# Kernel tuning notes

Hardware: AMD Instinct MI355X
Metric: run time of the kernel (lower is better)

The kernel has to match this reference:

```python
import jax, jax.numpy as jnp
import numpy as np

B, V, H = 4, 256, 128
EPS = 1e-5


def setup_inputs() -> dict:
    key = jax.random.key(0)
    ks = jax.random.split(key, 16)
    inp = {
        "h1": jax.random.normal(ks[0], (B, V, H), jnp.float32),
        "h2": jax.random.normal(ks[1], (B, V, H), jnp.float32),
        "e": jax.random.normal(ks[2], (B, V, V, H), jnp.float32),
        "graph": jax.random.randint(ks[3], (B, V, V), 0, 2, jnp.int32),
    }
    scale = 1.0 / np.sqrt(H)
    for i, nm in enumerate(["U1", "U2", "V1", "V2", "A1", "A2", "C"]):
        inp[f"W_{nm}"] = jax.random.normal(ks[4 + i], (H, H), jnp.float32) * scale
        inp[f"b_{nm}"] = jnp.zeros((H,), jnp.float32)
    for nm in ["h1", "h2", "e"]:
        inp[f"g_{nm}"] = jnp.ones((H,), jnp.float32)   # BN gamma
        inp[f"be_{nm}"] = jnp.zeros((H,), jnp.float32)  # BN beta
    return inp


def _lin(x, W, b):
    # torch nn.Linear: x @ W.T + b
    return jnp.einsum('...i,oi->...o', x, W) + b


def _bn(x, g, b):
    # BatchNorm1d with track_running_stats=False: batch stats over flattened leading dims
    sh = x.shape
    x2 = x.reshape(-1, sh[-1])
    m = x2.mean(axis=0)
    v = x2.var(axis=0)  # biased, as torch BN uses for normalization
    return ((x2 - m) * jax.lax.rsqrt(v + EPS) * g + b).reshape(sh)


def reference(h1, h2, e, graph,
              W_U1, b_U1, W_U2, b_U2, W_V1, b_V1, W_V2, b_V2,
              W_A1, b_A1, W_A2, b_A2, W_C, b_C,
              g_h1, be_h1, g_h2, be_h2, g_e, be_e):
    h1_in, h2_in, e_in = h1, h2, e

    Uh1 = _lin(h1, W_U1, b_U1)
    Uh2 = _lin(h2, W_U2, b_U2)
    Vh1 = _lin(h1, W_V1, b_V1)
    Vh2 = _lin(h2, W_V2, b_V2)

    # Wh1[b,i,j,h] = Vh1[b,j,h] + Vh2[b,i,h] ; Wh2 = transpose(1,2) pattern
    Wh1 = Vh1[:, None, :, :] + Vh2[:, :, None, :]
    Wh2 = Vh1[:, :, None, :] + Vh2[:, None, :, :]

    Ah1 = _lin(h1, W_A1, b_A1)
    Ah2 = _lin(h2, W_A2, b_A2)
    Ce = _lin(e, W_C, b_C)
    e_new = Ah1[:, None, :, :] + Ah2[:, :, None, :] + Ce  # B x V x V x H

    gates = jax.nn.sigmoid(e_new)
    gates_T = jax.nn.sigmoid(jnp.transpose(e_new, (0, 2, 1, 3)))

    # aggregation = 'sum' over dim 2 (graph unused for sum)
    h1n = Uh1 + jnp.sum(gates * Wh1, axis=2)
    h2n = Uh2 + jnp.sum(gates_T * Wh2, axis=2)

    h1n = jax.nn.relu(_bn(h1n, g_h1, be_h1))
    h2n = jax.nn.relu(_bn(h2n, g_h2, be_h2))
    e_out = jax.nn.relu(_bn(e_new, g_e, be_e))

    # mode == 'residual'
    return (h1_in + h1n, h2_in + h2n, e_in + e_out)
```

## Files before the change

### kernel.cpp

```cpp
#include <hip/hip_runtime.h>
#include <hip/hip_fp16.h>
#include <math.h>

#define BB 4
#define VV 256
#define HH 128
#define EPS 1e-5f

typedef __attribute__((ext_vector_type(8))) short short8;
typedef __attribute__((ext_vector_type(8))) __bf16 bf16x8;
typedef __attribute__((ext_vector_type(4))) float f32x4;

__device__ __forceinline__ float sigm_(float x) {
    float ex = __builtin_amdgcn_exp2f(-1.44269504f * x);
    return __builtin_amdgcn_rcpf(1.0f + ex);
}

__device__ __forceinline__ bf16x8 as_bf(short8 s) {
    union { short8 s; bf16x8 b; } u; u.s = s; return u.b;
}

__device__ __forceinline__ void split8n(const float4 x0, const float4 x1,
                                        bf16x8& hi, bf16x8& lo) {
    float xs[8] = {x0.x, x0.y, x0.z, x0.w, x1.x, x1.y, x1.z, x1.w};
    #pragma unroll
    for (int i = 0; i < 8; ++i) {
        float x = xs[i];
        __bf16 h = (__bf16)x;
        float r = x - (float)h;
        hi[i] = h;
        lo[i] = (__bf16)r;
    }
}

__global__ __launch_bounds__(256) void k0_splitW(const float* __restrict__ W_C,
                                                 short* __restrict__ Whl) {
    int t = blockIdx.x * 256 + threadIdx.x;
    int lane = t & 63;
    int grp = t >> 6;
    int kstep = grp >> 3, nsub = grp & 7;
    int n = (lane & 15) * 8 + nsub;
    int kb = kstep * 32 + ((lane >> 4) & 3) * 8;
    const float4* src = (const float4*)(W_C + (size_t)n * HH + kb);
    float4 x0 = src[0], x1 = src[1];
    bf16x8 hi, lo;
    split8n(x0, x1, hi, lo);
    union { bf16x8 b; short8 s; } uh, ul;
    uh.b = hi; ul.b = lo;
    short8* dst = (short8*)Whl;
    dst[(size_t)grp * 128 + 0 * 64 + lane] = uh.s;
    dst[(size_t)grp * 128 + 1 * 64 + lane] = ul.s;
}

struct LinArgs {
    const float* x1; const float* x2;
    const float* W[6]; const float* b[6]; const float* b2[6];
    float* out[6]; float* outf[6];
};

__global__ __launch_bounds__(128) void k1_linears(LinArgs a) {
    __shared__ float xs[2][8][HH];
    const int t = threadIdx.x;
    const int r0 = blockIdx.x * 8;
    {
        const float4* s1 = (const float4*)(a.x1 + (size_t)r0 * HH);
        const float4* s2 = (const float4*)(a.x2 + (size_t)r0 * HH);
        float4* d1 = (float4*)&xs[0][0][0];
        float4* d2 = (float4*)&xs[1][0][0];
        #pragma unroll
        for (int p = 0; p < 2; ++p) {
            d1[t + p * 128] = s1[t + p * 128];
            d2[t + p * 128] = s2[t + p * 128];
        }
    }
    __syncthreads();
    const int h = t;
    const int l15h = h >> 3, nsh = h & 7;
    for (int g = 0; g < 6; ++g) {
        const float* W = a.W[g];
        const float (*x)[HH] = (g < 3) ? xs[0] : xs[1];
        float acc[8];
        #pragma unroll
        for (int r = 0; r < 8; ++r) acc[r] = 0.f;
        const float4* Wrow = (const float4*)(W + (size_t)h * HH);
        #pragma unroll 8
        for (int kq = 0; kq < 32; ++kq) {
            float4 w4 = Wrow[kq];
            #pragma unroll
            for (int r = 0; r < 8; ++r) {
                float4 ev = *(const float4*)&x[r][kq * 4];
                acc[r] = fmaf(ev.x, w4.x, acc[r]);
                acc[r] = fmaf(ev.y, w4.y, acc[r]);
                acc[r] = fmaf(ev.z, w4.z, acc[r]);
                acc[r] = fmaf(ev.w, w4.w, acc[r]);
            }
        }
        float bias = a.b[g][h];
        if (a.b2[g]) bias += a.b2[g][h];
        if (a.out[g]) {
            float* O = a.out[g] + (size_t)r0 * HH + h;
            #pragma unroll
            for (int r = 0; r < 8; ++r) O[(size_t)r * HH] = acc[r] + bias;
        }
        if (a.outf[g]) {
            float* Of = a.outf[g];
            #pragma unroll
            for (int r = 0; r < 8; ++r)
                Of[((size_t)(r0 + r) * 16 + l15h) * 8 + nsh] = acc[r] + bias;
        }
    }
}

template<int STOREH>
__global__ __launch_bounds__(512, 4) void k2_main(
    const float* __restrict__ e,
    const short* __restrict__ Whl,
    const float* __restrict__ A1f, const float* __restrict__ A2f,
    const float* __restrict__ V1f, const float* __restrict__ V2f,
    float* __restrict__ e_new32,
    unsigned short* __restrict__ e_newh,
    float* __restrict__ h1acc,
    float* __restrict__ stats)
{
    __shared__ short8 sW[4096];
    __shared__ float red[8][3][8][16];
    const int t = threadIdx.x;
    const int l = t & 63;
    const int w = t >> 6;
    const int l15 = l & 15;
    const int lq = (l >> 4) & 3;
    const int blk = blockIdx.x;
    const int bi = blk >> 1;
    const int jhalf = blk & 1;
    const int b = bi >> 8;
    const int jbase = jhalf * 128 + w * 16;

    const float* pa = e + (size_t)bi * (VV * HH) +
                      (size_t)(jbase + l15) * HH + lq * 8;
    float4 ec[8];
    #pragma unroll
    for (int kstep = 0; kstep < 4; ++kstep) {
        ec[2 * kstep]     = *(const float4*)(pa + kstep * 32);
        ec[2 * kstep + 1] = *(const float4*)(pa + kstep * 32 + 4);
    }

    {
        const short8* src = (const short8*)Whl;
        #pragma unroll
        for (int p = 0; p < 8; ++p) sW[p * 512 + t] = src[p * 512 + t];
    }
    __syncthreads();

    f32x4 acc[8];
    #pragma unroll
    for (int ns = 0; ns < 8; ++ns) acc[ns] = (f32x4){0.f, 0.f, 0.f, 0.f};

    #pragma unroll
    for (int kstep = 0; kstep < 4; ++kstep) {
        bf16x8 ah, al;
        split8n(ec[2 * kstep], ec[2 * kstep + 1], ah, al);
        #pragma unroll
        for (int ns = 0; ns < 8; ++ns) {
            short8 bh = sW[(size_t)(kstep * 8 + ns) * 128 + l];
            short8 bl = sW[(size_t)(kstep * 8 + ns) * 128 + 64 + l];
            acc[ns] = __builtin_amdgcn_mfma_f32_16x16x32_bf16(
                ah, as_bf(bh), acc[ns], 0, 0, 0);
            acc[ns] = __builtin_amdgcn_mfma_f32_16x16x32_bf16(
                ah, as_bf(bl), acc[ns], 0, 0, 0);
            acc[ns] = __builtin_amdgcn_mfma_f32_16x16x32_bf16(
                al, as_bf(bh), acc[ns], 0, 0, 0);
        }
    }

    union f8u { float4 v[2]; float f[8]; };
    f8u a2, v2;
    {
        const float4* p = (const float4*)(A2f + ((size_t)bi * 16 + l15) * 8);
        a2.v[0] = p[0]; a2.v[1] = p[1];
        const float4* q = (const float4*)(V2f + ((size_t)bi * 16 + l15) * 8);
        v2.v[0] = q[0]; v2.v[1] = q[1];
    }
    float h1a[8], es[8], eq[8];
    #pragma unroll
    for (int ns = 0; ns < 8; ++ns) { h1a[ns] = 0.f; es[ns] = 0.f; eq[ns] = 0.f; }

    #pragma unroll
    for (int r = 0; r < 4; ++r) {
        int j = jbase + lq * 4 + r;
        size_t fro = ((size_t)(b * VV + j) * 16 + l15) * 8;
        f8u a1, v1;
        {
            const float4* p = (const float4*)(A1f + fro);
            a1.v[0] = p[0]; a1.v[1] = p[1];
            const float4* q = (const float4*)(V1f + fro);
            v1.v[0] = q[0]; v1.v[1] = q[1];
        }
        size_t obase = ((size_t)bi * VV + j) * HH + l15 * 8;
        float en8[8];
        #pragma unroll
        for (int ns = 0; ns < 8; ++ns) {
            float en = acc[ns][r] + a1.f[ns] + a2.f[ns];
            en8[ns] = en;
            float s = sigm_(en);
            h1a[ns] = fmaf(s, v1.f[ns] + v2.f[ns], h1a[ns]);
            es[ns] += en;
            eq[ns] = fmaf(en, en, eq[ns]);
        }
        if (STOREH) {
            union { __half2 h[4]; uint4 u; } pk;
            pk.h[0] = __floats2half2_rn(en8[0], en8[1]);
            pk.h[1] = __floats2half2_rn(en8[2], en8[3]);
            pk.h[2] = __floats2half2_rn(en8[4], en8[5]);
            pk.h[3] = __floats2half2_rn(en8[6], en8[7]);
            *(uint4*)(e_newh + obase) = pk.u;
        } else {
            float4 s0 = {en8[0], en8[1], en8[2], en8[3]};
            float4 s1 = {en8[4], en8[5], en8[6], en8[7]};
            *(float4*)(e_new32 + obase) = s0;
            *(float4*)(e_new32 + obase + 4) = s1;
        }
    }

    #pragma unroll
    for (int ns = 0; ns < 8; ++ns) {
        h1a[ns] += __shfl_xor(h1a[ns], 16);
        h1a[ns] += __shfl_xor(h1a[ns], 32);
        es[ns]  += __shfl_xor(es[ns], 16);
        es[ns]  += __shfl_xor(es[ns], 32);
        eq[ns]  += __shfl_xor(eq[ns], 16);
        eq[ns]  += __shfl_xor(eq[ns], 32);
    }
    if (l < 16) {
        #pragma unroll
        for (int ns = 0; ns < 8; ++ns) {
            red[w][0][ns][l15] = h1a[ns];
            red[w][1][ns][l15] = es[ns];
            red[w][2][ns][l15] = eq[ns];
        }
    }
    __syncthreads();
    if (t < 128) {
        int ns = t & 7, li = t >> 3;
        float h1t = 0.f, est = 0.f, eqt = 0.f;
        #pragma unroll
        for (int ww = 0; ww < 8; ++ww) {
            h1t += red[ww][0][ns][li];
            est += red[ww][1][ns][li];
            eqt += red[ww][2][ns][li];
        }
        atomicAdd(&h1acc[(size_t)bi * HH + t], h1t);
        atomicAdd(&stats[0 * HH + t], est);
        atomicAdd(&stats[1 * HH + t], eqt);
    }
}

template<int READH>
__global__ __launch_bounds__(256) void k4_pass2(
    float* __restrict__ e_io,
    const unsigned short* __restrict__ e_newh,
    const float* __restrict__ e_in,
    const float* __restrict__ V1, const float* __restrict__ V2,
    const float* __restrict__ g_e, const float* __restrict__ be_e,
    float* __restrict__ h2acc,
    const float* __restrict__ stats)
{
    const int t = threadIdx.x;
    const int h4 = (t & 31) * 4;
    const int jsub = t >> 5;
    const int blk = blockIdx.x;
    const int Iq = blk & 7;
    const int Jt = (blk >> 3) & 31;
    const int b = blk >> 8;
    const int J = Jt * 8 + jsub;
    const int bJ = (b << 8) + J;

    const float inv_n = 1.0f / (float)(BB * VV * VV);
    float sc[4], sh[4];
    #pragma unroll
    for (int c = 0; c < 4; ++c) {
        int h = h4 + c;
        float mean = stats[0 * HH + h] * inv_n;
        float var  = stats[1 * HH + h] * inv_n - mean * mean;
        float rstd = rsqrtf(var + EPS);
        sc[c] = rstd * g_e[h];
        sh[c] = be_e[h] - mean * sc[c];
    }
    float4 vh1 = *(const float4*)(V1 + (size_t)bJ * HH + h4);
    float4 h2a = {0.f, 0.f, 0.f, 0.f};

    const int I0beg = Iq * 32;
    for (int I0 = I0beg; I0 < I0beg + 32; I0 += 4) {
        float4 en[4], ei[4], v2[4];
        size_t off[4];
        #pragma unroll
        for (int u = 0; u < 4; ++u) {
            int I = I0 + u;
            off[u] = ((size_t)((b * VV + I) * VV) + J) * HH + h4;
            if (READH) {
                ushort4 eh = *(const ushort4*)(e_newh + off[u]);
                en[u].x = __half2float(__ushort_as_half(eh.x));
                en[u].y = __half2float(__ushort_as_half(eh.y));
                en[u].z = __half2float(__ushort_as_half(eh.z));
                en[u].w = __half2float(__ushort_as_half(eh.w));
            } else {
                en[u] = *(const float4*)(e_io + off[u]);
            }
            ei[u] = *(const float4*)(e_in + off[u]);
            v2[u] = *(const float4*)(V2 + (size_t)((b << 8) + I) * HH + h4);
        }
        #pragma unroll
        for (int u = 0; u < 4; ++u) {
            float4 r;
            float* enf = (float*)&en[u];
            float* eif = (float*)&ei[u];
            float* v2f = (float*)&v2[u];
            float* rf = (float*)&r;
            float* h2f = (float*)&h2a;
            float* v1f = (float*)&vh1;
            #pragma unroll
            for (int c = 0; c < 4; ++c) {
                float e_ = enf[c];
                h2f[c] = fmaf(sigm_(e_), v1f[c] + v2f[c], h2f[c]);
                float bn = fmaf(e_, sc[c], sh[c]);
                rf[c] = eif[c] + fmaxf(bn, 0.f);
            }
            *(float4*)(e_io + off[u]) = r;
        }
    }
    float* base = h2acc + (size_t)bJ * HH + h4;
    float* h2f = (float*)&h2a;
    #pragma unroll
    for (int c = 0; c < 4; ++c) atomicAdd(base + c, h2f[c]);
}

__global__ __launch_bounds__(256) void k45_combine(
    float* __restrict__ h1acc, float* __restrict__ h2acc,
    const float* __restrict__ U1, const float* __restrict__ U2,
    float* __restrict__ stats)
{
    __shared__ float red[2][2][128];
    const int t = threadIdx.x;
    const int h = t & 127;
    const int rr = t >> 7;
    const int region = blockIdx.x >> 5;
    const int r0 = (blockIdx.x & 31) * 32;
    float* acc = region ? h2acc : h1acc;
    const float* U = region ? U2 : U1;
    float s = 0.f, q = 0.f;
    #pragma unroll
    for (int rs = 0; rs < 16; ++rs) {
        size_t idx = (size_t)(r0 + rr * 16 + rs) * HH + h;
        float v = acc[idx] + U[idx];
        acc[idx] = v;
        s += v;
        q = fmaf(v, v, q);
    }
    red[0][rr][h] = s;
    red[1][rr][h] = q;
    __syncthreads();
    if (t < 128) {
        atomicAdd(&stats[(2 + 2 * region) * HH + h], red[0][0][h] + red[0][1][h]);
        atomicAdd(&stats[(3 + 2 * region) * HH + h], red[1][0][h] + red[1][1][h]);
    }
}

__global__ __launch_bounds__(256) void k5_final(
    const float* __restrict__ h1_in, const float* __restrict__ h2_in,
    const float* __restrict__ h1p, const float* __restrict__ h2p,
    const float* __restrict__ g1, const float* __restrict__ be1,
    const float* __restrict__ g2, const float* __restrict__ be2,
    float* __restrict__ out,
    const float* __restrict__ stats)
{
    const float inv_n = 1.0f / 1024.0f;
    int idx0 = blockIdx.x * 2048 + threadIdx.x;
    #pragma unroll
    for (int p = 0; p < 8; ++p) {
        int idx = idx0 + p * 256;
        int region = idx >> 17;
        int local = idx & 131071;
        int h = idx & 127;
        float ssum = stats[(2 + 2 * region) * HH + h];
        float ssq  = stats[(3 + 2 * region) * HH + h];
        float mean = ssum * inv_n;
        float var  = ssq * inv_n - mean * mean;
        float rstd = rsqrtf(var + EPS);
        const float* g  = region ? g2 : g1;
        const float* be = region ? be2 : be1;
        float sc = rstd * g[h];
        float sh = be[h] - mean * sc;
        const float* xin = region ? h2_in : h1_in;
        const float* pre = region ? h2p : h1p;
        out[idx] = xin[local] + fmaxf(fmaf(pre[local], sc, sh), 0.f);
    }
}

extern "C" void kernel_launch(void* const* d_in, const int* in_sizes, int n_in,
                              void* d_out, int out_size, void* d_ws, size_t ws_size,
                              hipStream_t stream) {
    const float* h1   = (const float*)d_in[0];
    const float* h2   = (const float*)d_in[1];
    const float* e    = (const float*)d_in[2];
    const float* W_U1 = (const float*)d_in[4];
    const float* b_U1 = (const float*)d_in[5];
    const float* W_U2 = (const float*)d_in[6];
    const float* b_U2 = (const float*)d_in[7];
    const float* W_V1 = (const float*)d_in[8];
    const float* b_V1 = (const float*)d_in[9];
    const float* W_V2 = (const float*)d_in[10];
    const float* b_V2 = (const float*)d_in[11];
    const float* W_A1 = (const float*)d_in[12];
    const float* b_A1 = (const float*)d_in[13];
    const float* W_A2 = (const float*)d_in[14];
    const float* b_A2 = (const float*)d_in[15];
    const float* W_C  = (const float*)d_in[16];
    const float* b_C  = (const float*)d_in[17];
    const float* g_h1 = (const float*)d_in[18];
    const float* be_h1= (const float*)d_in[19];
    const float* g_h2 = (const float*)d_in[20];
    const float* be_h2= (const float*)d_in[21];
    const float* g_e  = (const float*)d_in[22];
    const float* be_e = (const float*)d_in[23];

    float* ws = (float*)d_ws;
    const size_t S = (size_t)BB * VV * HH;
    float* U1  = ws + 0 * S;
    float* U2  = ws + 1 * S;
    float* V1  = ws + 2 * S;
    float* V2  = ws + 3 * S;
    float* V1f = ws + 4 * S;
    float* V2f = ws + 5 * S;
    float* A1f = ws + 6 * S;
    float* A2f = ws + 7 * S;
    float* h1acc = ws + 8 * S;
    float* h2acc = ws + 9 * S;
    float* stats = ws + 10 * S;
    short* Whl  = (short*)(stats + 768);
    unsigned short* e_newh = (unsigned short*)(Whl + 32768);

    const size_t EN = (size_t)BB * VV * VV * HH;
    const size_t needed = (10 * S + 768) * 4 + 65536 + EN * 2;
    const bool useh = ws_size >= needed;

    float* out = (float*)d_out;
    float* eo = out + 2 * S;

    hipMemsetAsync(h1acc, 0, (2 * S + 768) * sizeof(float), stream);

    k0_splitW<<<8, 256, 0, stream>>>(W_C, Whl);

    LinArgs la;
    la.x1 = h1; la.x2 = h2;
    la.W[0] = W_U1; la.b[0] = b_U1; la.b2[0] = nullptr; la.out[0] = U1; la.outf[0] = nullptr;
    la.W[1] = W_V1; la.b[1] = b_V1; la.b2[1] = nullptr; la.out[1] = V1; la.outf[1] = V1f;
    la.W[2] = W_A1; la.b[2] = b_A1; la.b2[2] = b_C;     la.out[2] = nullptr; la.outf[2] = A1f;
    la.W[3] = W_U2; la.b[3] = b_U2; la.b2[3] = nullptr; la.out[3] = U2; la.outf[3] = nullptr;
    la.W[4] = W_V2; la.b[4] = b_V2; la.b2[4] = nullptr; la.out[4] = V2; la.outf[4] = V2f;
    la.W[5] = W_A2; la.b[5] = b_A2; la.b2[5] = nullptr; la.out[5] = nullptr; la.outf[5] = A2f;
    k1_linears<<<128, 128, 0, stream>>>(la);

    if (useh) {
        k2_main<1><<<BB * VV * 2, 512, 0, stream>>>(e, Whl, A1f, A2f, V1f, V2f,
                                                    eo, e_newh, h1acc, stats);
        k4_pass2<1><<<BB * 32 * 8, 256, 0, stream>>>(eo, e_newh, e, V1, V2,
                                                     g_e, be_e, h2acc, stats);
    } else {
        k2_main<0><<<BB * VV * 2, 512, 0, stream>>>(e, Whl, A1f, A2f, V1f, V2f,
                                                    eo, e_newh, h1acc, stats);
        k4_pass2<0><<<BB * 32 * 8, 256, 0, stream>>>(eo, e_newh, e, V1, V2,
                                                     g_e, be_e, h2acc, stats);
    }

    k45_combine<<<64, 256, 0, stream>>>(h1acc, h2acc, U1, U2, stats);

    k5_final<<<128, 256, 0, stream>>>(h1, h2, h1acc, h2acc,
                                      g_h1, be_h1, g_h2, be_h2, out, stats);
}
```

Before: 188.3 us.

## Fold memset, weight split and h1 combine into neighbouring kernels

Removes the memset and the separate W_C hi/lo split launch by folding both into the linear-projection kernel, with extra blocks doing the split and every thread doing a grid-stride zero fill. The h1 residual/stat combine moves into spare blocks of the pass-2 kernel, so only the h2 combine remains as its own launch. The k2 MFMA loop also raises wave priority with s_setprio. This cuts launch count and per-launch overhead. The zero fill now runs inside the same kernel as other work that writes elsewhere, so ordering depends only on the kernel boundary before k2.

```diff
diff --git a/kernel.cpp b/kernel.cpp
--- a/kernel.cpp
+++ b/kernel.cpp
@@ -33,35 +33,45 @@
     }
 }
 
-__global__ __launch_bounds__(256) void k0_splitW(const float* __restrict__ W_C,
-                                                 short* __restrict__ Whl) {
-    int t = blockIdx.x * 256 + threadIdx.x;
-    int lane = t & 63;
-    int grp = t >> 6;
-    int kstep = grp >> 3, nsub = grp & 7;
-    int n = (lane & 15) * 8 + nsub;
-    int kb = kstep * 32 + ((lane >> 4) & 3) * 8;
-    const float4* src = (const float4*)(W_C + (size_t)n * HH + kb);
-    float4 x0 = src[0], x1 = src[1];
-    bf16x8 hi, lo;
-    split8n(x0, x1, hi, lo);
-    union { bf16x8 b; short8 s; } uh, ul;
-    uh.b = hi; ul.b = lo;
-    short8* dst = (short8*)Whl;
-    dst[(size_t)grp * 128 + 0 * 64 + lane] = uh.s;
-    dst[(size_t)grp * 128 + 1 * 64 + lane] = ul.s;
-}
-
 struct LinArgs {
     const float* x1; const float* x2;
     const float* W[6]; const float* b[6]; const float* b2[6];
     float* out[6]; float* outf[6];
 };
 
-__global__ __launch_bounds__(128) void k1_linears(LinArgs a) {
+__global__ __launch_bounds__(128) void k1_fused(LinArgs a,
+                                                const float* __restrict__ W_C,
+                                                short* __restrict__ Whl,
+                                                float4* __restrict__ zbase,
+                                                int nz4) {
+    const int blk = blockIdx.x;
+    const int tid = threadIdx.x;
+    {
+        int gtid = blk * 128 + tid;
+        float4 z = {0.f, 0.f, 0.f, 0.f};
+        for (int i = gtid; i < nz4; i += 144 * 128) zbase[i] = z;
+    }
+    if (blk >= 128) {
+        int t = (blk - 128) * 128 + tid;
+        int lane = t & 63;
+        int grp = t >> 6;
+        int kstep = grp >> 3, nsub = grp & 7;
+        int n = (lane & 15) * 8 + nsub;
+        int kb = kstep * 32 + ((lane >> 4) & 3) * 8;
+        const float4* src = (const float4*)(W_C + (size_t)n * HH + kb);
+        float4 x0 = src[0], x1 = src[1];
+        bf16x8 hi, lo;
+        split8n(x0, x1, hi, lo);
+        union { bf16x8 b; short8 s; } uh, ul;
+        uh.b = hi; ul.b = lo;
+        short8* dst = (short8*)Whl;
+        dst[(size_t)grp * 128 + 0 * 64 + lane] = uh.s;
+        dst[(size_t)grp * 128 + 1 * 64 + lane] = ul.s;
+        return;
+    }
     __shared__ float xs[2][8][HH];
-    const int t = threadIdx.x;
-    const int r0 = blockIdx.x * 8;
+    const int t = tid;
+    const int r0 = blk * 8;
     {
         const float4* s1 = (const float4*)(a.x1 + (size_t)r0 * HH);
         const float4* s2 = (const float4*)(a.x2 + (size_t)r0 * HH);
@@ -155,6 +165,7 @@
     #pragma unroll
     for (int ns = 0; ns < 8; ++ns) acc[ns] = (f32x4){0.f, 0.f, 0.f, 0.f};
 
+    __builtin_amdgcn_s_setprio(1);
     #pragma unroll
     for (int kstep = 0; kstep < 4; ++kstep) {
         bf16x8 ah, al;
@@ -171,6 +182,7 @@
                 al, as_bf(bh), acc[ns], 0, 0, 0);
         }
     }
+    __builtin_amdgcn_s_setprio(0);
 
     union f8u { float4 v[2]; float f[8]; };
     f8u a2, v2;
@@ -262,12 +274,39 @@
     const float* __restrict__ V1, const float* __restrict__ V2,
     const float* __restrict__ g_e, const float* __restrict__ be_e,
     float* __restrict__ h2acc,
-    const float* __restrict__ stats)
+    float* __restrict__ h1acc, const float* __restrict__ U1,
+    float* __restrict__ stats)
 {
+    __shared__ float red[2][2][128];
     const int t = threadIdx.x;
+    const int blk = blockIdx.x;
+
+    if (blk >= 1024) {
+        const int rb = blk - 1024;
+        const int h = t & 127;
+        const int rr = t >> 7;
+        const int r0 = rb * 32;
+        float s = 0.f, q = 0.f;
+        #pragma unroll
+        for (int rs = 0; rs < 16; ++rs) {
+            size_t idx = (size_t)(r0 + rr * 16 + rs) * HH + h;
+            float v = h1acc[idx] + U1[idx];
+            h1acc[idx] = v;
+            s += v;
+            q = fmaf(v, v, q);
+        }
+        red[0][rr][h] = s;
+        red[1][rr][h] = q;
+        __syncthreads();
+        if (t < 128) {
+            atomicAdd(&stats[2 * HH + h], red[0][0][h] + red[0][1][h]);
+            atomicAdd(&stats[3 * HH + h], red[1][0][h] + red[1][1][h]);
+        }
+        return;
+    }
+
     const int h4 = (t & 31) * 4;
     const int jsub = t >> 5;
-    const int blk = blockIdx.x;
     const int Iq = blk & 7;
     const int Jt = (blk >> 3) & 31;
     const int b = blk >> 8;
@@ -333,25 +372,21 @@
     for (int c = 0; c < 4; ++c) atomicAdd(base + c, h2f[c]);
 }
 
-__global__ __launch_bounds__(256) void k45_combine(
-    float* __restrict__ h1acc, float* __restrict__ h2acc,
-    const float* __restrict__ U1, const float* __restrict__ U2,
+__global__ __launch_bounds__(256) void k45_h2(
+    float* __restrict__ h2acc, const float* __restrict__ U2,
     float* __restrict__ stats)
 {
     __shared__ float red[2][2][128];
     const int t = threadIdx.x;
     const int h = t & 127;
     const int rr = t >> 7;
-    const int region = blockIdx.x >> 5;
-    const int r0 = (blockIdx.x & 31) * 32;
-    float* acc = region ? h2acc : h1acc;
-    const float* U = region ? U2 : U1;
+    const int r0 = blockIdx.x * 32;
     float s = 0.f, q = 0.f;
     #pragma unroll
     for (int rs = 0; rs < 16; ++rs) {
         size_t idx = (size_t)(r0 + rr * 16 + rs) * HH + h;
-        float v = acc[idx] + U[idx];
-        acc[idx] = v;
+        float v = h2acc[idx] + U2[idx];
+        h2acc[idx] = v;
         s += v;
         q = fmaf(v, v, q);
     }
@@ -359,8 +394,8 @@
     red[1][rr][h] = q;
     __syncthreads();
     if (t < 128) {
-        atomicAdd(&stats[(2 + 2 * region) * HH + h], red[0][0][h] + red[0][1][h]);
-        atomicAdd(&stats[(3 + 2 * region) * HH + h], red[1][0][h] + red[1][1][h]);
+        atomicAdd(&stats[4 * HH + h], red[0][0][h] + red[0][1][h]);
+        atomicAdd(&stats[5 * HH + h], red[1][0][h] + red[1][1][h]);
     }
 }
 
@@ -445,9 +480,7 @@
     float* out = (float*)d_out;
     float* eo = out + 2 * S;
 
-    hipMemsetAsync(h1acc, 0, (2 * S + 768) * sizeof(float), stream);
-
-    k0_splitW<<<8, 256, 0, stream>>>(W_C, Whl);
+    const int nz4 = (int)((2 * S + 768) / 4);
 
     LinArgs la;
     la.x1 = h1; la.x2 = h2;
@@ -457,21 +490,23 @@
     la.W[3] = W_U2; la.b[3] = b_U2; la.b2[3] = nullptr; la.out[3] = U2; la.outf[3] = nullptr;
     la.W[4] = W_V2; la.b[4] = b_V2; la.b2[4] = nullptr; la.out[4] = V2; la.outf[4] = V2f;
     la.W[5] = W_A2; la.b[5] = b_A2; la.b2[5] = nullptr; la.out[5] = nullptr; la.outf[5] = A2f;
-    k1_linears<<<128, 128, 0, stream>>>(la);
+    k1_fused<<<144, 128, 0, stream>>>(la, W_C, Whl, (float4*)h1acc, nz4);
 
     if (useh) {
         k2_main<1><<<BB * VV * 2, 512, 0, stream>>>(e, Whl, A1f, A2f, V1f, V2f,
                                                     eo, e_newh, h1acc, stats);
-        k4_pass2<1><<<BB * 32 * 8, 256, 0, stream>>>(eo, e_newh, e, V1, V2,
-                                                     g_e, be_e, h2acc, stats);
+        k4_pass2<1><<<1024 + 32, 256, 0, stream>>>(eo, e_newh, e, V1, V2,
+                                                   g_e, be_e, h2acc,
+                                                   h1acc, U1, stats);
     } else {
         k2_main<0><<<BB * VV * 2, 512, 0, stream>>>(e, Whl, A1f, A2f, V1f, V2f,
                                                     eo, e_newh, h1acc, stats);
-        k4_pass2<0><<<BB * 32 * 8, 256, 0, stream>>>(eo, e_newh, e, V1, V2,
-                                                     g_e, be_e, h2acc, stats);
-    }
-
-    k45_combine<<<64, 256, 0, stream>>>(h1acc, h2acc, U1, U2, stats);
+        k4_pass2<0><<<1024 + 32, 256, 0, stream>>>(eo, e_newh, e, V1, V2,
+                                                   g_e, be_e, h2acc,
+                                                   h1acc, U1, stats);
+    }
+
+    k45_h2<<<32, 256, 0, stream>>>(h2acc, U2, stats);
 
     k5_final<<<128, 256, 0, stream>>>(h1, h2, h1acc, h2acc,
                                       g_h1, be_h1, g_h2, be_h2, out, stats);
```

Result: no change. 187.1 us (-0.6%).
